# Optimization experiments

Hardware: AMD Instinct MI355X
Metric: run time of the kernel (lower is better)

## Reference

```python
import jax, jax.numpy as jnp
import numpy as np

N_NODES = 100000
N_EDGES = 3200000
D_FEAT = 128


def setup_inputs() -> dict:
    key = jax.random.key(0)
    k1, k2, k3, k4 = jax.random.split(key, 4)
    edge_row = jax.random.randint(k1, (N_EDGES,), 0, N_NODES, dtype=jnp.int64 if jax.config.jax_enable_x64 else jnp.int32)
    edge_col = jax.random.randint(k2, (N_EDGES,), 0, N_NODES, dtype=edge_row.dtype)
    edge_val = jax.random.uniform(k3, (N_EDGES,), dtype=jnp.float32)
    embeds = jax.random.normal(k4, (N_NODES, D_FEAT), dtype=jnp.float32)
    return {"edge_row": edge_row, "edge_col": edge_col, "edge_val": edge_val, "embeds": embeds}


def reference(edge_row, edge_col, edge_val, embeds):
    # SpMM: out[r] = sum_{e: row(e)=r} val(e) * embeds[col(e)]
    messages = edge_val[:, None] * embeds[edge_col]  # [E, D]
    out = jax.ops.segment_sum(messages, edge_row, num_segments=embeds.shape[0])  # [N, D]
    return out
```

## Files before the change

### kernel.cpp

```cpp
#include <hip/hip_runtime.h>
#include <stdint.h>

#define N_NODES 100000
#define D_FEAT  128
#define RSH     5
#define RPB     32
#define NBUCK   ((N_NODES + RPB - 1) / RPB)
#define CAPF    1152
#define KMAX    ((CAPF + 255) / 256)
#define OCAP    8192
#define SC_THR  1024
#define SC_EPT  8
#define SC_TILE (SC_THR * SC_EPT)
#define COLMASK 0x1FFFF

__global__ __launch_bounds__(SC_THR) void scatter_fixed_kernel(
    const int* __restrict__ row, const int* __restrict__ col,
    const float* __restrict__ val, int* __restrict__ cursor,
    int2* __restrict__ rec, int4* __restrict__ oflow, int* __restrict__ ocnt, int n,
    const uint64_t* __restrict__ embin, uint32_t* __restrict__ embbf, int do_conv,
    int cpad)
{
    __shared__ int cnt[NBUCK];
    __shared__ int base[NBUCK];
    const int tid = threadIdx.x;

    if (do_conv) {
        const int n2 = N_NODES * (D_FEAT / 2);
        const int stride = (int)gridDim.x * SC_THR;
        for (int i = (int)blockIdx.x * SC_THR + tid; i < n2; i += stride) {
            uint64_t u = __builtin_nontemporal_load(embin + i);
            uint32_t bx = (uint32_t)u, by = (uint32_t)(u >> 32);
            bx = (bx + 0x7FFFu + ((bx >> 16) & 1u)) >> 16;
            by = (by + 0x7FFFu + ((by >> 16) & 1u)) >> 16;
            embbf[i] = bx | (by << 16);
        }
    }

    const int e0 = (int)blockIdx.x * SC_TILE + tid * SC_EPT;

    for (int i = tid; i < NBUCK; i += SC_THR) cnt[i] = 0;
    __syncthreads();

    int   r[SC_EPT], c[SC_EPT];
    float v[SC_EPT];
    if (e0 + SC_EPT <= n) {
        const int4* rp = (const int4*)(row + e0);
        const int4* cp = (const int4*)(col + e0);
        const float4* vp = (const float4*)(val + e0);
        #pragma unroll
        for (int q = 0; q < SC_EPT / 4; q++) {
            int4 rr = rp[q]; int4 cc = cp[q]; float4 vv = vp[q];
            r[q*4+0]=rr.x; r[q*4+1]=rr.y; r[q*4+2]=rr.z; r[q*4+3]=rr.w;
            c[q*4+0]=cc.x; c[q*4+1]=cc.y; c[q*4+2]=cc.z; c[q*4+3]=cc.w;
            v[q*4+0]=vv.x; v[q*4+1]=vv.y; v[q*4+2]=vv.z; v[q*4+3]=vv.w;
        }
    } else {
        #pragma unroll
        for (int k = 0; k < SC_EPT; k++) {
            int e = e0 + k;
            if (e < n) { r[k] = row[e]; c[k] = col[e]; v[k] = val[e]; }
            else       { r[k] = -1; }
        }
    }

    int rk[SC_EPT];
    #pragma unroll
    for (int k = 0; k < SC_EPT; k++)
        if (r[k] >= 0) rk[k] = atomicAdd(&cnt[r[k] >> RSH], 1);
    __syncthreads();

    for (int i = tid; i < NBUCK; i += SC_THR) {
        int cc = cnt[i];
        if (cc) base[i] = atomicAdd(&cursor[(size_t)i * cpad], cc);
    }
    __syncthreads();

    #pragma unroll
    for (int k = 0; k < SC_EPT; k++) {
        if (r[k] >= 0) {
            int bk  = r[k] >> RSH;
            int pos = base[bk] + rk[k];
            if (pos < CAPF) {
                rec[(size_t)bk * CAPF + pos] =
                    make_int2(((r[k] & (RPB - 1)) << 17) | c[k], __float_as_int(v[k]));
            } else {
                int op = atomicAdd(ocnt, 1);
                if (op < OCAP) oflow[op] = make_int4(r[k], c[k], __float_as_int(v[k]), 0);
            }
        }
    }
}

template <bool BF16>
__global__ __launch_bounds__(256, 8) void spmm_fixed_kernel(const int* __restrict__ fill,
                                                            const int2* __restrict__ rec,
                                                            const void* __restrict__ emb,
                                                            float* __restrict__ out,
                                                            int cpad)
{
    __shared__ int2 buf[CAPF];
    __shared__ int  cnt[RPB];
    __shared__ int  start[RPB];
    __shared__ int  sc_[RPB];

    const int tid  = threadIdx.x;
    const int lane = tid & 63;
    const int wv   = tid >> 6;
    const int b    = blockIdx.x;
    const int m    = min(fill[(size_t)b * cpad], CAPF);
    const uint64_t* __restrict__ rec8 = (const uint64_t*)rec + (size_t)b * CAPF;
    const uint32_t* __restrict__ embu = (const uint32_t*)emb;
    const float2*   __restrict__ emb2 = (const float2*)emb;

    if (tid < RPB) cnt[tid] = 0;
    __syncthreads();

    int2 rc[KMAX];
    int  rk[KMAX];
    #pragma unroll
    for (int k = 0; k < KMAX; k++) {
        int i = k * 256 + tid;
        if (i < m) {
            uint64_t u = __builtin_nontemporal_load(rec8 + i);
            rc[k].x = (int)(uint32_t)u;
            rc[k].y = (int)(uint32_t)(u >> 32);
            rk[k] = atomicAdd(&cnt[(uint32_t)rc[k].x >> 17], 1);
        }
    }
    __syncthreads();
    if (tid < RPB) sc_[tid] = cnt[tid];
    __syncthreads();
    for (int off = 1; off < RPB; off <<= 1) {
        int t = 0;
        if (tid < RPB && tid >= off) t = sc_[tid - off];
        __syncthreads();
        if (tid < RPB) sc_[tid] += t;
        __syncthreads();
    }
    if (tid < RPB) start[tid] = sc_[tid] - cnt[tid];
    __syncthreads();
    #pragma unroll
    for (int k = 0; k < KMAX; k++) {
        int i = k * 256 + tid;
        if (i < m) buf[start[(uint32_t)rc[k].x >> 17] + rk[k]] = rc[k];
    }
    __syncthreads();

    for (int rl = wv * 8; rl < wv * 8 + 8; rl++) {
        const int s0 = start[rl];
        const int c0 = cnt[rl];
        float ax = 0.f, ay = 0.f;
        int j = 0;
        for (; j + 16 <= c0; j += 16) {
            uint32_t u[16]; float vv[16]; float2 m2[16];
            #pragma unroll
            for (int q = 0; q < 16; q++) {
                int2 e = buf[s0 + j + q];
                u[q]  = (((uint32_t)e.x & COLMASK) << 6) | (uint32_t)lane;
                vv[q] = __int_as_float(e.y);
            }
            #pragma unroll
            for (int q = 0; q < 16; q++) {
                if (BF16) u[q] = embu[u[q]]; else m2[q] = emb2[u[q]];
            }
            #pragma unroll
            for (int q = 0; q < 16; q++) {
                if (BF16) {
                    ax += vv[q] * __uint_as_float(u[q] << 16);
                    ay += vv[q] * __uint_as_float(u[q] & 0xFFFF0000u);
                } else {
                    ax += vv[q] * m2[q].x; ay += vv[q] * m2[q].y;
                }
            }
        }
        for (; j + 4 <= c0; j += 4) {
            uint32_t u[4]; float vv[4]; float2 m2[4];
            #pragma unroll
            for (int q = 0; q < 4; q++) {
                int2 e = buf[s0 + j + q];
                u[q]  = (((uint32_t)e.x & COLMASK) << 6) | (uint32_t)lane;
                vv[q] = __int_as_float(e.y);
            }
            #pragma unroll
            for (int q = 0; q < 4; q++) {
                if (BF16) u[q] = embu[u[q]]; else m2[q] = emb2[u[q]];
            }
            #pragma unroll
            for (int q = 0; q < 4; q++) {
                if (BF16) {
                    ax += vv[q] * __uint_as_float(u[q] << 16);
                    ay += vv[q] * __uint_as_float(u[q] & 0xFFFF0000u);
                } else {
                    ax += vv[q] * m2[q].x; ay += vv[q] * m2[q].y;
                }
            }
        }
        for (; j < c0; j++) {
            int2 e = buf[s0 + j];
            uint32_t off = (((uint32_t)e.x & COLMASK) << 6) | (uint32_t)lane;
            float vv = __int_as_float(e.y);
            if (BF16) {
                uint32_t u = embu[off];
                ax += vv * __uint_as_float(u << 16);
                ay += vv * __uint_as_float(u & 0xFFFF0000u);
            } else {
                float2 mm = emb2[off];
                ax += vv * mm.x; ay += vv * mm.y;
            }
        }
        const int grow = b * RPB + rl;
        uint64_t w = (uint64_t)__float_as_uint(ax) | ((uint64_t)__float_as_uint(ay) << 32);
        __builtin_nontemporal_store(w, (uint64_t*)out + (size_t)grow * 64 + lane);
    }
}

__global__ __launch_bounds__(256) void oflow_kernel(const int4* __restrict__ oflow,
                                                    const int* __restrict__ ocnt,
                                                    const float* __restrict__ embeds,
                                                    float* __restrict__ out) {
    const int nof  = min(*ocnt, OCAP);
    const int lane = threadIdx.x & 63;
    const int w    = ((int)blockIdx.x * 256 + threadIdx.x) >> 6;
    const int nw   = ((int)gridDim.x * 256) >> 6;
    for (int i = w; i < nof; i += nw) {
        int4 e = oflow[i];
        const float2* src = (const float2*)(embeds + (size_t)e.y * D_FEAT);
        float2 mm = src[lane];
        float vv = __int_as_float(e.z);
        float* dst = out + (size_t)e.x * D_FEAT + (lane << 1);
        unsafeAtomicAdd(dst,     vv * mm.x);
        unsafeAtomicAdd(dst + 1, vv * mm.y);
    }
}

__global__ __launch_bounds__(256) void spmm_atomic_kernel(
    const int* __restrict__ edge_row, const int* __restrict__ edge_col,
    const float* __restrict__ edge_val, const float* __restrict__ embeds,
    float* __restrict__ out, int n_edges)
{
    const int lane    = threadIdx.x & 63;
    const int wave_id = ((int)blockIdx.x * blockDim.x + threadIdx.x) >> 6;
    const int n_waves = ((int)gridDim.x * blockDim.x) >> 6;
    for (int e = wave_id; e < n_edges; e += n_waves) {
        const int   r = edge_row[e];
        const int   c = edge_col[e];
        const float vv = edge_val[e];
        const float2* src = (const float2*)(embeds + (size_t)c * D_FEAT);
        float2 mm = src[lane];
        float* dst = out + (size_t)r * D_FEAT + (lane << 1);
        unsafeAtomicAdd(dst,     vv * mm.x);
        unsafeAtomicAdd(dst + 1, vv * mm.y);
    }
}

static inline size_t align256(size_t x) { return (x + 255) & ~(size_t)255; }

extern "C" void kernel_launch(void* const* d_in, const int* in_sizes, int n_in,
                              void* d_out, int out_size, void* d_ws, size_t ws_size,
                              hipStream_t stream) {
    const int*   edge_row = (const int*)d_in[0];
    const int*   edge_col = (const int*)d_in[1];
    const float* edge_val = (const float*)d_in[2];
    const float* embeds   = (const float*)d_in[3];
    float*       out      = (float*)d_out;

    const int n_edges = in_sizes[0];

    const size_t cur16  = align256(((size_t)NBUCK * 16 + 16) * 4);
    const size_t cur1   = align256(((size_t)NBUCK + 16) * 4);
    const size_t of_sz  = align256((size_t)OCAP * 16);
    const size_t rec_sz = align256((size_t)NBUCK * CAPF * 8);
    const size_t emb_sz = align256((size_t)N_NODES * 64 * 4);

    int  cpad;
    bool use_bf16;
    size_t cur_sz;
    if (ws_size >= cur16 + of_sz + rec_sz + emb_sz)      { cpad = 16; use_bf16 = true;  cur_sz = cur16; }
    else if (ws_size >= cur1 + of_sz + rec_sz + emb_sz)  { cpad = 1;  use_bf16 = true;  cur_sz = cur1;  }
    else if (ws_size >= cur1 + of_sz + rec_sz)           { cpad = 1;  use_bf16 = false; cur_sz = cur1;  }
    else {
        hipMemsetAsync(out, 0, (size_t)out_size * sizeof(float), stream);
        spmm_atomic_kernel<<<dim3(4096), dim3(256), 0, stream>>>(
            edge_row, edge_col, edge_val, embeds, out, n_edges);
        return;
    }

    char* ws = (char*)d_ws;
    int*      cursor = (int*)ws;
    int*      ocnt   = cursor + (size_t)NBUCK * cpad;
    int4*     oflow  = (int4*)(ws + cur_sz);
    int2*     rec    = (int2*)(ws + cur_sz + of_sz);
    uint32_t* embbf  = (uint32_t*)(ws + cur_sz + of_sz + rec_sz);

    hipMemsetAsync(cursor, 0, ((size_t)NBUCK * cpad + 1) * 4, stream);
    scatter_fixed_kernel<<<dim3((n_edges + SC_TILE - 1) / SC_TILE), dim3(SC_THR), 0, stream>>>(
        edge_row, edge_col, edge_val, cursor, rec, oflow, ocnt, n_edges,
        (const uint64_t*)embeds, embbf, use_bf16 ? 1 : 0, cpad);
    if (use_bf16)
        spmm_fixed_kernel<true><<<dim3(NBUCK), dim3(256), 0, stream>>>(cursor, rec, embbf, out, cpad);
    else
        spmm_fixed_kernel<false><<<dim3(NBUCK), dim3(256), 0, stream>>>(cursor, rec, embeds, out, cpad);
    oflow_kernel<<<dim3(16), dim3(256), 0, stream>>>(oflow, ocnt, embeds, out);
}
```

Baseline: 308.3 us.

## Double scatter bucket size and split each bucket across two SpMM blocks

Scatter buckets now cover 64 rows instead of 32, which halves the number of buckets and cursor atomics in the scatter phase. The SpMM launch doubles its grid so that each block reads the whole 64-row bucket but keeps only the 32 rows of its half. Each bucket's records are therefore read twice, and each block now holds a register array twice as large. Adds a bounds check on output rows.

Measured after the change: 287.6 us. -6.7%, faster.

```diff
diff --git a/kernel.cpp b/kernel.cpp
--- a/kernel.cpp
+++ b/kernel.cpp
@@ -3,11 +3,12 @@
 
 #define N_NODES 100000
 #define D_FEAT  128
-#define RSH     5
-#define RPB     32
+#define RSH     6
+#define RPB     64
 #define NBUCK   ((N_NODES + RPB - 1) / RPB)
-#define CAPF    1152
+#define CAPF    2304
 #define KMAX    ((CAPF + 255) / 256)
+#define HROWS   32
 #define OCAP    8192
 #define SC_THR  1024
 #define SC_EPT  8
@@ -100,20 +101,21 @@
                                                             int cpad)
 {
     __shared__ int2 buf[CAPF];
-    __shared__ int  cnt[RPB];
-    __shared__ int  start[RPB];
-    __shared__ int  sc_[RPB];
+    __shared__ int  cnt[HROWS];
+    __shared__ int  start[HROWS];
+    __shared__ int  sc_[HROWS];
 
     const int tid  = threadIdx.x;
     const int lane = tid & 63;
     const int wv   = tid >> 6;
-    const int b    = blockIdx.x;
+    const int b    = blockIdx.x >> 1;
+    const int half = blockIdx.x & 1;
     const int m    = min(fill[(size_t)b * cpad], CAPF);
     const uint64_t* __restrict__ rec8 = (const uint64_t*)rec + (size_t)b * CAPF;
     const uint32_t* __restrict__ embu = (const uint32_t*)emb;
     const float2*   __restrict__ emb2 = (const float2*)emb;
 
-    if (tid < RPB) cnt[tid] = 0;
+    if (tid < HROWS) cnt[tid] = 0;
     __syncthreads();
 
     int2 rc[KMAX];
@@ -121,29 +123,32 @@
     #pragma unroll
     for (int k = 0; k < KMAX; k++) {
         int i = k * 256 + tid;
+        rk[k] = -1;
         if (i < m) {
             uint64_t u = __builtin_nontemporal_load(rec8 + i);
             rc[k].x = (int)(uint32_t)u;
             rc[k].y = (int)(uint32_t)(u >> 32);
-            rk[k] = atomicAdd(&cnt[(uint32_t)rc[k].x >> 17], 1);
-        }
-    }
-    __syncthreads();
-    if (tid < RPB) sc_[tid] = cnt[tid];
-    __syncthreads();
-    for (int off = 1; off < RPB; off <<= 1) {
+            int rl6 = (int)((uint32_t)rc[k].x >> 17);
+            if ((rl6 >> 5) == half)
+                rk[k] = atomicAdd(&cnt[rl6 & (HROWS - 1)], 1);
+        }
+    }
+    __syncthreads();
+    if (tid < HROWS) sc_[tid] = cnt[tid];
+    __syncthreads();
+    for (int off = 1; off < HROWS; off <<= 1) {
         int t = 0;
-        if (tid < RPB && tid >= off) t = sc_[tid - off];
+        if (tid < HROWS && tid >= off) t = sc_[tid - off];
         __syncthreads();
-        if (tid < RPB) sc_[tid] += t;
+        if (tid < HROWS) sc_[tid] += t;
         __syncthreads();
     }
-    if (tid < RPB) start[tid] = sc_[tid] - cnt[tid];
+    if (tid < HROWS) start[tid] = sc_[tid] - cnt[tid];
     __syncthreads();
     #pragma unroll
     for (int k = 0; k < KMAX; k++) {
-        int i = k * 256 + tid;
-        if (i < m) buf[start[(uint32_t)rc[k].x >> 17] + rk[k]] = rc[k];
+        if (rk[k] >= 0)
+            buf[start[((uint32_t)rc[k].x >> 17) & (HROWS - 1)] + rk[k]] = rc[k];
     }
     __syncthreads();
 
@@ -209,9 +214,11 @@
                 ax += vv * mm.x; ay += vv * mm.y;
             }
         }
-        const int grow = b * RPB + rl;
-        uint64_t w = (uint64_t)__float_as_uint(ax) | ((uint64_t)__float_as_uint(ay) << 32);
-        __builtin_nontemporal_store(w, (uint64_t*)out + (size_t)grow * 64 + lane);
+        const int grow = b * RPB + half * HROWS + rl;
+        if (grow < N_NODES) {
+            uint64_t w = (uint64_t)__float_as_uint(ax) | ((uint64_t)__float_as_uint(ay) << 32);
+            __builtin_nontemporal_store(w, (uint64_t*)out + (size_t)grow * 64 + lane);
+        }
     }
 }
 
@@ -298,8 +305,8 @@
         edge_row, edge_col, edge_val, cursor, rec, oflow, ocnt, n_edges,
         (const uint64_t*)embeds, embbf, use_bf16 ? 1 : 0, cpad);
     if (use_bf16)
-        spmm_fixed_kernel<true><<<dim3(NBUCK), dim3(256), 0, stream>>>(cursor, rec, embbf, out, cpad);
+        spmm_fixed_kernel<true><<<dim3(NBUCK * 2), dim3(256), 0, stream>>>(cursor, rec, embbf, out, cpad);
     else
-        spmm_fixed_kernel<false><<<dim3(NBUCK), dim3(256), 0, stream>>>(cursor, rec, embeds, out, cpad);
+        spmm_fixed_kernel<false><<<dim3(NBUCK * 2), dim3(256), 0, stream>>>(cursor, rec, embeds, out, cpad);
     oflow_kernel<<<dim3(16), dim3(256), 0, stream>>>(oflow, ocnt, embeds, out);
 }
```
